# Optimization experiments

Measured on AMD Instinct MI355X. Metric: run time of the kernel, lower is better.

## Reference

```python
import jax, jax.numpy as jnp
import numpy as np

B, C, H, W, P = 16, 512, 64, 64, 32


def setup_inputs() -> dict:
    key = jax.random.key(0)
    k1, k2, k3 = jax.random.split(key, 3)
    inputs = jax.random.normal(k1, (B, C, H, W), dtype=jnp.float32)
    weight = jax.random.uniform(k2, (P, C, 1, 1), dtype=jnp.float32)
    smooth_factor = jax.random.normal(k3, (P,), dtype=jnp.float32)
    return {"inputs": inputs, "weight": weight, "smooth_factor": smooth_factor}


def reference(inputs, weight, smooth_factor):
    b, c, h, w = inputs.shape
    p = weight.shape[0]
    n = h * w
    centers = weight.reshape(p, c)                      # [P,C]
    x = inputs.reshape(b, c, n)                         # [B,C,N]

    # distance-based logits: 2<c,x> - |x|^2 - |c|^2, clamped at 0
    cx = jnp.einsum('pc,bcn->bpn', centers, x)          # [B,P,N]
    x_sq = jnp.sum(x * x, axis=1, keepdims=True)        # [B,1,N]
    c_sq = jnp.sum(centers * centers, axis=1)[None, :, None]  # [1,P,1]
    beta = jax.nn.sigmoid(smooth_factor)                # [P]
    logits = jnp.minimum(2.0 * cx - x_sq - c_sq, 0.0) / beta[None, :, None]
    assign = jax.nn.softmax(logits, axis=1)             # [B,P,N]

    # assignment-weighted pooling
    qx = jnp.einsum('bpn,bcn->bpc', assign, x)          # [B,P,C]
    sum_ass = jnp.clip(jnp.sum(assign, axis=2, keepdims=True), 1e-5)  # [B,P,1]
    sigma = jnp.sqrt(beta / 2.0)                        # [P]
    out = (qx / sum_ass - centers[None, :, :]) / sigma[None, :, None]

    # L2-normalize over channel dim (torch F.normalize, eps=1e-12)
    norm = jnp.sqrt(jnp.sum(out * out, axis=2, keepdims=True))
    outputs = out / jnp.maximum(norm, 1e-12)
    outputs_t = jnp.transpose(outputs, (0, 2, 1))       # [B,C,P]
    assign_map = assign.reshape(b, p, h, w)             # [B,P,H,W]
    return outputs_t, assign_map
```

## Files before the change

### kernel.cpp

```cpp
#include <hip/hip_runtime.h>

constexpr int BB = 16;
constexpr int CC = 512;
constexpr int PP = 32;
constexpr int NN = 4096;

using f32x4 = __attribute__((ext_vector_type(4))) float;
using bf16x8 = __attribute__((ext_vector_type(8))) short;
typedef unsigned int uint;

__device__ __forceinline__ ushort f2bf(float f) {
  unsigned u = __builtin_bit_cast(unsigned, f);
  u += 0x7FFFu + ((u >> 16) & 1u);
  return (ushort)(u >> 16);
}

__global__ __launch_bounds__(64) void prep_kernel(
    const float* __restrict__ w, const float* __restrict__ sf,
    float* __restrict__ beta, float* __restrict__ rbeta,
    float* __restrict__ csq, float* __restrict__ zbase,
    ushort* __restrict__ chi, ushort* __restrict__ clo) {
  int p = blockIdx.x;
  int t = threadIdx.x;
  float4* z4 = (float4*)zbase;
  for (int i = blockIdx.x * 64 + t; i < 65664; i += 32 * 64)
    z4[i] = make_float4(0.f, 0.f, 0.f, 0.f);

  float s = 0.f;
  int c8 = t * 8;
  float4 v0 = *(const float4*)&w[p * CC + c8];
  float4 v1 = *(const float4*)&w[p * CC + c8 + 4];
  ushort h[8], l[8];
  float vv[8] = {v0.x, v0.y, v0.z, v0.w, v1.x, v1.y, v1.z, v1.w};
#pragma unroll
  for (int i = 0; i < 8; ++i) {
    s = fmaf(vv[i], vv[i], s);
    h[i] = f2bf(vv[i]);
    float hf = __builtin_bit_cast(float, (uint)h[i] << 16);
    l[i] = f2bf(vv[i] - hf);
  }
  *(ushort4*)&chi[p * CC + c8] = make_ushort4(h[0], h[1], h[2], h[3]);
  *(ushort4*)&chi[p * CC + c8 + 4] = make_ushort4(h[4], h[5], h[6], h[7]);
  *(ushort4*)&clo[p * CC + c8] = make_ushort4(l[0], l[1], l[2], l[3]);
  *(ushort4*)&clo[p * CC + c8 + 4] = make_ushort4(l[4], l[5], l[6], l[7]);
#pragma unroll
  for (int off = 32; off; off >>= 1) s += __shfl_down(s, off);
  if (t == 0) {
    csq[p] = s;
    float e = __expf(-sf[p]);
    rbeta[p] = 1.f + e;
    beta[p] = 1.f / (1.f + e);
  }
}

__global__ __launch_bounds__(256) void assign_kernel(
    const float* __restrict__ x, const ushort* __restrict__ chi,
    const ushort* __restrict__ clo, const float* __restrict__ rbeta_,
    const float* __restrict__ csq_, float* __restrict__ assign_out,
    float* __restrict__ sum_ass) {
  int tid = threadIdx.x;
  int wv = tid >> 6, lane = tid & 63;
  int l15 = lane & 15, lg = lane >> 4;
  int b = blockIdx.x >> 5;
  int n0 = (blockIdx.x & 31) * 128 + wv * 32;

  const float* xb = x + (size_t)b * CC * NN + n0 + l15;

  f32x4 acc[2][2];
#pragma unroll
  for (int i = 0; i < 2; ++i)
#pragma unroll
    for (int j = 0; j < 2; ++j) acc[i][j] = {0.f, 0.f, 0.f, 0.f};
  float xsq[2] = {0.f, 0.f};

#pragma unroll 4
  for (int ks = 0; ks < 16; ++ks) {
    int c0 = ks * 32 + lg * 8;
    bf16x8 Ah0 = *(const bf16x8*)&chi[l15 * CC + c0];
    bf16x8 Ah1 = *(const bf16x8*)&chi[(l15 + 16) * CC + c0];
    bf16x8 Al0 = *(const bf16x8*)&clo[l15 * CC + c0];
    bf16x8 Al1 = *(const bf16x8*)&clo[(l15 + 16) * CC + c0];
#pragma unroll
    for (int nf = 0; nf < 2; ++nf) {
      float xv[8];
#pragma unroll
      for (int j = 0; j < 8; ++j)
        xv[j] = xb[(size_t)(c0 + j) * NN + nf * 16];
      union { bf16x8 v; ushort e[8]; } Bh, Bl;
#pragma unroll
      for (int j = 0; j < 8; ++j) {
        xsq[nf] = fmaf(xv[j], xv[j], xsq[nf]);
        ushort h = f2bf(xv[j]);
        float hf = __builtin_bit_cast(float, (uint)h << 16);
        Bh.e[j] = h;
        Bl.e[j] = f2bf(xv[j] - hf);
      }
      acc[0][nf] = __builtin_amdgcn_mfma_f32_16x16x32_bf16(Ah0, Bh.v, acc[0][nf], 0, 0, 0);
      acc[1][nf] = __builtin_amdgcn_mfma_f32_16x16x32_bf16(Ah1, Bh.v, acc[1][nf], 0, 0, 0);
      acc[0][nf] = __builtin_amdgcn_mfma_f32_16x16x32_bf16(Ah0, Bl.v, acc[0][nf], 0, 0, 0);
      acc[1][nf] = __builtin_amdgcn_mfma_f32_16x16x32_bf16(Ah1, Bl.v, acc[1][nf], 0, 0, 0);
      acc[0][nf] = __builtin_amdgcn_mfma_f32_16x16x32_bf16(Al0, Bh.v, acc[0][nf], 0, 0, 0);
      acc[1][nf] = __builtin_amdgcn_mfma_f32_16x16x32_bf16(Al1, Bh.v, acc[1][nf], 0, 0, 0);
    }
  }

#pragma unroll
  for (int nf = 0; nf < 2; ++nf) {
    xsq[nf] += __shfl_xor(xsq[nf], 16);
    xsq[nf] += __shfl_xor(xsq[nf], 32);
  }

  float csqv[2][4], rbv[2][4];
#pragma unroll
  for (int pf = 0; pf < 2; ++pf)
#pragma unroll
    for (int i = 0; i < 4; ++i) {
      int p = pf * 16 + lg * 4 + i;
      csqv[pf][i] = csq_[p];
      rbv[pf][i] = rbeta_[p];
    }

  float L[2][2][4];
  float m[2] = {-3.4e38f, -3.4e38f};
#pragma unroll
  for (int pf = 0; pf < 2; ++pf)
#pragma unroll
    for (int nf = 0; nf < 2; ++nf)
#pragma unroll
      for (int i = 0; i < 4; ++i) {
        float l = fminf(2.f * acc[pf][nf][i] - xsq[nf] - csqv[pf][i], 0.f) * rbv[pf][i];
        L[pf][nf][i] = l;
        m[nf] = fmaxf(m[nf], l);
      }
#pragma unroll
  for (int nf = 0; nf < 2; ++nf) {
    m[nf] = fmaxf(m[nf], __shfl_xor(m[nf], 16));
    m[nf] = fmaxf(m[nf], __shfl_xor(m[nf], 32));
  }
  float s[2] = {0.f, 0.f};
#pragma unroll
  for (int pf = 0; pf < 2; ++pf)
#pragma unroll
    for (int nf = 0; nf < 2; ++nf)
#pragma unroll
      for (int i = 0; i < 4; ++i) {
        float e = __expf(L[pf][nf][i] - m[nf]);
        L[pf][nf][i] = e;
        s[nf] += e;
      }
#pragma unroll
  for (int nf = 0; nf < 2; ++nf) {
    s[nf] += __shfl_xor(s[nf], 16);
    s[nf] += __shfl_xor(s[nf], 32);
    s[nf] = 1.f / s[nf];
  }

  float* aoB = assign_out + (size_t)b * PP * NN + n0 + l15;
#pragma unroll
  for (int pf = 0; pf < 2; ++pf)
#pragma unroll
    for (int i = 0; i < 4; ++i) {
      int p = pf * 16 + lg * 4 + i;
      float a0 = L[pf][0][i] * s[0];
      float a1 = L[pf][1][i] * s[1];
      aoB[(size_t)p * NN] = a0;
      aoB[(size_t)p * NN + 16] = a1;
      float v = a0 + a1;
      v += __shfl_xor(v, 1); v += __shfl_xor(v, 2);
      v += __shfl_xor(v, 4); v += __shfl_xor(v, 8);
      if (l15 == 0) atomicAdd(&sum_ass[b * PP + p], v);
    }
}

__global__ __launch_bounds__(256, 4) void qx_kernel(
    const float* __restrict__ x, const float* __restrict__ assign,
    float* __restrict__ qx) {
  int tid = threadIdx.x;
  int wv = tid >> 6, lane = tid & 63;
  int l15 = lane & 15, lg = lane >> 4;
  int b = blockIdx.y;
  int ct = blockIdx.x >> 2;
  int kc = (blockIdx.x & 3) * 4 + wv;

  const float* ab = assign + (size_t)b * PP * NN + kc * 256;
  const float* xb = x + ((size_t)b * CC + ct * 32) * NN + kc * 256;

  f32x4 q[2][2];
#pragma unroll
  for (int i = 0; i < 2; ++i)
#pragma unroll
    for (int j = 0; j < 2; ++j) q[i][j] = {0.f, 0.f, 0.f, 0.f};

#pragma unroll 2
  for (int ks = 0; ks < 8; ++ks) {
    int ko = ks * 32 + lg * 8;
    union { bf16x8 v; ushort e[8]; } A0, A1;
    {
      const float* ar = &ab[(size_t)l15 * NN + ko];
      float4 u0 = *(const float4*)ar;
      float4 u1 = *(const float4*)(ar + 4);
      A0.e[0] = f2bf(u0.x); A0.e[1] = f2bf(u0.y);
      A0.e[2] = f2bf(u0.z); A0.e[3] = f2bf(u0.w);
      A0.e[4] = f2bf(u1.x); A0.e[5] = f2bf(u1.y);
      A0.e[6] = f2bf(u1.z); A0.e[7] = f2bf(u1.w);
      const float* ar1 = &ab[(size_t)(l15 + 16) * NN + ko];
      float4 w0 = *(const float4*)ar1;
      float4 w1 = *(const float4*)(ar1 + 4);
      A1.e[0] = f2bf(w0.x); A1.e[1] = f2bf(w0.y);
      A1.e[2] = f2bf(w0.z); A1.e[3] = f2bf(w0.w);
      A1.e[4] = f2bf(w1.x); A1.e[5] = f2bf(w1.y);
      A1.e[6] = f2bf(w1.z); A1.e[7] = f2bf(w1.w);
    }
#pragma unroll
    for (int cf = 0; cf < 2; ++cf) {
      const float* xr = &xb[(size_t)(cf * 16 + l15) * NN + ko];
      float4 u0 = *(const float4*)xr;
      float4 u1 = *(const float4*)(xr + 4);
      union { bf16x8 v; ushort e[8]; } Bv;
      Bv.e[0] = f2bf(u0.x); Bv.e[1] = f2bf(u0.y);
      Bv.e[2] = f2bf(u0.z); Bv.e[3] = f2bf(u0.w);
      Bv.e[4] = f2bf(u1.x); Bv.e[5] = f2bf(u1.y);
      Bv.e[6] = f2bf(u1.z); Bv.e[7] = f2bf(u1.w);
      q[0][cf] = __builtin_amdgcn_mfma_f32_16x16x32_bf16(A0.v, Bv.v, q[0][cf], 0, 0, 0);
      q[1][cf] = __builtin_amdgcn_mfma_f32_16x16x32_bf16(A1.v, Bv.v, q[1][cf], 0, 0, 0);
    }
  }

#pragma unroll
  for (int pf = 0; pf < 2; ++pf)
#pragma unroll
    for (int cf = 0; cf < 2; ++cf)
#pragma unroll
      for (int i = 0; i < 4; ++i) {
        int p = pf * 16 + lg * 4 + i;
        int c = ct * 32 + cf * 16 + l15;
        atomicAdd(&qx[((size_t)b * PP + p) * CC + c], q[pf][cf][i]);
      }
}

__global__ __launch_bounds__(256) void finalize_kernel(
    const float* __restrict__ qx, const float* __restrict__ w,
    const float* __restrict__ beta, const float* __restrict__ sum_ass,
    float* __restrict__ out_t) {
  int b = blockIdx.x >> 5;
  int p = blockIdx.x & 31;
  int tid = threadIdx.x;
  int wave = tid >> 6, lane = tid & 63;

  float inv_sa = 1.f / fmaxf(sum_ass[b * PP + p], 1e-5f);
  float rsig = rsqrtf(0.5f * beta[p]);

  int c0 = tid, c1 = tid + 256;
  const float* qrow = qx + ((size_t)b * PP + p) * CC;
  const float* wrow = w + (size_t)p * CC;
  float t0 = (qrow[c0] * inv_sa - wrow[c0]) * rsig;
  float t1 = (qrow[c1] * inv_sa - wrow[c1]) * rsig;

  float nr = t0 * t0 + t1 * t1;
#pragma unroll
  for (int off = 32; off; off >>= 1) nr += __shfl_down(nr, off);
  __shared__ float red[4];
  if (lane == 0) red[wave] = nr;
  __syncthreads();
  float norm2 = red[0] + red[1] + red[2] + red[3];
  float scale = 1.f / fmaxf(sqrtf(norm2), 1e-12f);

  float* ob = out_t + (size_t)b * CC * PP + p;
  ob[(size_t)c0 * PP] = t0 * scale;
  ob[(size_t)c1 * PP] = t1 * scale;
}

extern "C" void kernel_launch(void* const* d_in, const int* in_sizes, int n_in,
                              void* d_out, int out_size, void* d_ws,
                              size_t ws_size, hipStream_t stream) {
  const float* x = (const float*)d_in[0];
  const float* w = (const float*)d_in[1];
  const float* sf = (const float*)d_in[2];

  float* out_t = (float*)d_out;
  float* assign = out_t + (size_t)BB * CC * PP;

  float* ws = (float*)d_ws;
  float* beta = ws;
  float* rbeta = ws + 32;
  float* csq = ws + 64;
  float* sum_ass = ws + 96;
  float* qx = ws + 608;
  ushort* chi = (ushort*)(ws + 608 + 262144);
  ushort* clo = chi + PP * CC;

  prep_kernel<<<PP, 64, 0, stream>>>(w, sf, beta, rbeta, csq, sum_ass,
                                     chi, clo);
  assign_kernel<<<512, 256, 0, stream>>>(x, chi, clo, rbeta, csq, assign,
                                         sum_ass);
  qx_kernel<<<dim3(64, BB), 256, 0, stream>>>(x, assign, qx);
  finalize_kernel<<<BB * PP, 256, 0, stream>>>(qx, w, beta, sum_ass, out_t);
}
```

Before: 93.07 us.

## Fuse qx pooling into assign kernel using LDS bf16 assignments and partial buffers

Each assign block now writes its bf16 assignment tile to shared memory and immediately computes that tile's contribution to qx against x. This removes the separate qx kernel and its re-read of the assign output from global memory. Atomic contention is spread over 8 partial qx buffers that finalize sums, and prep now zeroes a larger workspace with more blocks. The trade-offs are re-reading x for the pooling step inside a 512-block grid (possibly lower parallelism than the old 1024-block qx kernel), more atomics per block, and a larger zeroing pass.

```diff
diff --git a/kernel.cpp b/kernel.cpp
--- a/kernel.cpp
+++ b/kernel.cpp
@@ -20,12 +20,13 @@
     float* __restrict__ beta, float* __restrict__ rbeta,
     float* __restrict__ csq, float* __restrict__ zbase,
     ushort* __restrict__ chi, ushort* __restrict__ clo) {
-  int p = blockIdx.x;
   int t = threadIdx.x;
   float4* z4 = (float4*)zbase;
-  for (int i = blockIdx.x * 64 + t; i < 65664; i += 32 * 64)
+  for (int i = blockIdx.x * 64 + t; i < 524416; i += 256 * 64)
     z4[i] = make_float4(0.f, 0.f, 0.f, 0.f);
 
+  if (blockIdx.x >= PP) return;
+  int p = blockIdx.x;
   float s = 0.f;
   int c8 = t * 8;
   float4 v0 = *(const float4*)&w[p * CC + c8];
@@ -53,16 +54,20 @@
   }
 }
 
-__global__ __launch_bounds__(256) void assign_kernel(
+__global__ __launch_bounds__(256) void fused_kernel(
     const float* __restrict__ x, const ushort* __restrict__ chi,
     const ushort* __restrict__ clo, const float* __restrict__ rbeta_,
     const float* __restrict__ csq_, float* __restrict__ assign_out,
-    float* __restrict__ sum_ass) {
+    float* __restrict__ sum_ass, float* __restrict__ qx_part) {
+  __shared__ ushort albf[PP][136];
+
   int tid = threadIdx.x;
   int wv = tid >> 6, lane = tid & 63;
   int l15 = lane & 15, lg = lane >> 4;
   int b = blockIdx.x >> 5;
-  int n0 = (blockIdx.x & 31) * 128 + wv * 32;
+  int ntile = blockIdx.x & 31;
+  int n0blk = ntile * 128;
+  int n0 = n0blk + wv * 32;
 
   const float* xb = x + (size_t)b * CC * NN + n0 + l15;
 
@@ -165,81 +170,62 @@
       float a1 = L[pf][1][i] * s[1];
       aoB[(size_t)p * NN] = a0;
       aoB[(size_t)p * NN + 16] = a1;
+      albf[p][wv * 32 + l15] = f2bf(a0);
+      albf[p][wv * 32 + 16 + l15] = f2bf(a1);
       float v = a0 + a1;
       v += __shfl_xor(v, 1); v += __shfl_xor(v, 2);
       v += __shfl_xor(v, 4); v += __shfl_xor(v, 8);
       if (l15 == 0) atomicAdd(&sum_ass[b * PP + p], v);
     }
-}
-
-__global__ __launch_bounds__(256, 4) void qx_kernel(
-    const float* __restrict__ x, const float* __restrict__ assign,
-    float* __restrict__ qx) {
-  int tid = threadIdx.x;
-  int wv = tid >> 6, lane = tid & 63;
-  int l15 = lane & 15, lg = lane >> 4;
-  int b = blockIdx.y;
-  int ct = blockIdx.x >> 2;
-  int kc = (blockIdx.x & 3) * 4 + wv;
-
-  const float* ab = assign + (size_t)b * PP * NN + kc * 256;
-  const float* xb = x + ((size_t)b * CC + ct * 32) * NN + kc * 256;
-
-  f32x4 q[2][2];
-#pragma unroll
-  for (int i = 0; i < 2; ++i)
-#pragma unroll
-    for (int j = 0; j < 2; ++j) q[i][j] = {0.f, 0.f, 0.f, 0.f};
-
-#pragma unroll 2
-  for (int ks = 0; ks < 8; ++ks) {
-    int ko = ks * 32 + lg * 8;
-    union { bf16x8 v; ushort e[8]; } A0, A1;
-    {
-      const float* ar = &ab[(size_t)l15 * NN + ko];
-      float4 u0 = *(const float4*)ar;
-      float4 u1 = *(const float4*)(ar + 4);
-      A0.e[0] = f2bf(u0.x); A0.e[1] = f2bf(u0.y);
-      A0.e[2] = f2bf(u0.z); A0.e[3] = f2bf(u0.w);
-      A0.e[4] = f2bf(u1.x); A0.e[5] = f2bf(u1.y);
-      A0.e[6] = f2bf(u1.z); A0.e[7] = f2bf(u1.w);
-      const float* ar1 = &ab[(size_t)(l15 + 16) * NN + ko];
-      float4 w0 = *(const float4*)ar1;
-      float4 w1 = *(const float4*)(ar1 + 4);
-      A1.e[0] = f2bf(w0.x); A1.e[1] = f2bf(w0.y);
-      A1.e[2] = f2bf(w0.z); A1.e[3] = f2bf(w0.w);
-      A1.e[4] = f2bf(w1.x); A1.e[5] = f2bf(w1.y);
-      A1.e[6] = f2bf(w1.z); A1.e[7] = f2bf(w1.w);
-    }
-#pragma unroll
-    for (int cf = 0; cf < 2; ++cf) {
-      const float* xr = &xb[(size_t)(cf * 16 + l15) * NN + ko];
-      float4 u0 = *(const float4*)xr;
-      float4 u1 = *(const float4*)(xr + 4);
-      union { bf16x8 v; ushort e[8]; } Bv;
-      Bv.e[0] = f2bf(u0.x); Bv.e[1] = f2bf(u0.y);
-      Bv.e[2] = f2bf(u0.z); Bv.e[3] = f2bf(u0.w);
-      Bv.e[4] = f2bf(u1.x); Bv.e[5] = f2bf(u1.y);
-      Bv.e[6] = f2bf(u1.z); Bv.e[7] = f2bf(u1.w);
-      q[0][cf] = __builtin_amdgcn_mfma_f32_16x16x32_bf16(A0.v, Bv.v, q[0][cf], 0, 0, 0);
-      q[1][cf] = __builtin_amdgcn_mfma_f32_16x16x32_bf16(A1.v, Bv.v, q[1][cf], 0, 0, 0);
-    }
-  }
-
-#pragma unroll
-  for (int pf = 0; pf < 2; ++pf)
-#pragma unroll
-    for (int cf = 0; cf < 2; ++cf)
-#pragma unroll
-      for (int i = 0; i < 4; ++i) {
-        int p = pf * 16 + lg * 4 + i;
-        int c = ct * 32 + cf * 16 + l15;
-        atomicAdd(&qx[((size_t)b * PP + p) * CC + c], q[pf][cf][i]);
-      }
+
+  __syncthreads();
+
+  const float* xg = x + (size_t)b * CC * NN + n0blk;
+  float* qp = qx_part + (size_t)(ntile & 7) * BB * PP * CC +
+              (size_t)b * PP * CC;
+
+#pragma unroll
+  for (int chalf = 0; chalf < 2; ++chalf) {
+    int cbase = wv * 128 + chalf * 64;
+    f32x4 q[2][4];
+#pragma unroll
+    for (int pf = 0; pf < 2; ++pf)
+#pragma unroll
+      for (int cf = 0; cf < 4; ++cf) q[pf][cf] = {0.f, 0.f, 0.f, 0.f};
+#pragma unroll
+    for (int ks = 0; ks < 4; ++ks) {
+      int ko = ks * 32 + lg * 8;
+      bf16x8 A0 = *(const bf16x8*)&albf[l15][ko];
+      bf16x8 A1 = *(const bf16x8*)&albf[l15 + 16][ko];
+#pragma unroll
+      for (int cf = 0; cf < 4; ++cf) {
+        const float* xr = &xg[(size_t)(cbase + cf * 16 + l15) * NN + ko];
+        float4 u0 = *(const float4*)xr;
+        float4 u1 = *(const float4*)(xr + 4);
+        union { bf16x8 v; ushort e[8]; } Bv;
+        Bv.e[0] = f2bf(u0.x); Bv.e[1] = f2bf(u0.y);
+        Bv.e[2] = f2bf(u0.z); Bv.e[3] = f2bf(u0.w);
+        Bv.e[4] = f2bf(u1.x); Bv.e[5] = f2bf(u1.y);
+        Bv.e[6] = f2bf(u1.z); Bv.e[7] = f2bf(u1.w);
+        q[0][cf] = __builtin_amdgcn_mfma_f32_16x16x32_bf16(A0, Bv.v, q[0][cf], 0, 0, 0);
+        q[1][cf] = __builtin_amdgcn_mfma_f32_16x16x32_bf16(A1, Bv.v, q[1][cf], 0, 0, 0);
+      }
+    }
+#pragma unroll
+    for (int pf = 0; pf < 2; ++pf)
+#pragma unroll
+      for (int cf = 0; cf < 4; ++cf)
+#pragma unroll
+        for (int i = 0; i < 4; ++i) {
+          int p = pf * 16 + lg * 4 + i;
+          int c = cbase + cf * 16 + l15;
+          atomicAdd(&qp[(size_t)p * CC + c], q[pf][cf][i]);
+        }
+  }
 }
 
 __global__ __launch_bounds__(256) void finalize_kernel(
-    const float* __restrict__ qx, const float* __restrict__ w,
+    const float* __restrict__ qx_part, const float* __restrict__ w,
     const float* __restrict__ beta, const float* __restrict__ sum_ass,
     float* __restrict__ out_t) {
   int b = blockIdx.x >> 5;
@@ -251,10 +237,16 @@
   float rsig = rsqrtf(0.5f * beta[p]);
 
   int c0 = tid, c1 = tid + 256;
-  const float* qrow = qx + ((size_t)b * PP + p) * CC;
+  float q0 = 0.f, q1 = 0.f;
+#pragma unroll
+  for (int kc = 0; kc < 8; ++kc) {
+    const float* row = qx_part + (((size_t)kc * BB + b) * PP + p) * CC;
+    q0 += row[c0];
+    q1 += row[c1];
+  }
   const float* wrow = w + (size_t)p * CC;
-  float t0 = (qrow[c0] * inv_sa - wrow[c0]) * rsig;
-  float t1 = (qrow[c1] * inv_sa - wrow[c1]) * rsig;
+  float t0 = (q0 * inv_sa - wrow[c0]) * rsig;
+  float t1 = (q1 * inv_sa - wrow[c1]) * rsig;
 
   float nr = t0 * t0 + t1 * t1;
 #pragma unroll
@@ -285,14 +277,14 @@
   float* rbeta = ws + 32;
   float* csq = ws + 64;
   float* sum_ass = ws + 96;
-  float* qx = ws + 608;
-  ushort* chi = (ushort*)(ws + 608 + 262144);
+  float* qx_part = ws + 608;
+  ushort* chi = (ushort*)(ws + 608 + 2097152);
   ushort* clo = chi + PP * CC;
 
-  prep_kernel<<<PP, 64, 0, stream>>>(w, sf, beta, rbeta, csq, sum_ass,
-                                     chi, clo);
-  assign_kernel<<<512, 256, 0, stream>>>(x, chi, clo, rbeta, csq, assign,
-                                         sum_ass);
-  qx_kernel<<<dim3(64, BB), 256, 0, stream>>>(x, assign, qx);
-  finalize_kernel<<<BB * PP, 256, 0, stream>>>(qx, w, beta, sum_ass, out_t);
-}
+  prep_kernel<<<256, 64, 0, stream>>>(w, sf, beta, rbeta, csq, sum_ass,
+                                      chi, clo);
+  fused_kernel<<<BB * 32, 256, 0, stream>>>(x, chi, clo, rbeta, csq,
+                                            assign, sum_ass, qx_part);
+  finalize_kernel<<<BB * PP, 256, 0, stream>>>(qx_part, w, beta, sum_ass,
+                                               out_t);
+}
```

Result: faster. 86.09 us (-7.5%).
